# Optimization experiments

Measured on AMD Instinct MI355X. Metric: run time of the kernel, lower is better.

Reference implementation:

```python
import jax, jax.numpy as jnp
import numpy as np

DIM = 1024
D_STATE = 16

def setup_inputs() -> dict:
    key = jax.random.key(0)
    kx, ka, kd = jax.random.split(key, 3)
    x = jax.random.normal(kx, (4, 8192, DIM), dtype=jnp.float32)
    A = jax.random.normal(ka, (DIM, D_STATE), dtype=jnp.float32)
    D = jax.random.normal(kd, (D_STATE, DIM), dtype=jnp.float32)
    return {"x": x, "A": A, "D": D}

def reference(x, A, D):
    # x: [B, N, C]; A: [C, S]; D: [S, C]
    x_state = jnp.einsum('bnc,cs->bns', x, A)        # [B, N, S]
    x_state = jnp.cumsum(x_state, axis=1)            # prefix sum over sequence
    out = jnp.einsum('bns,sc->bnc', x_state, D)      # [B, N, C]
    return out
```

## Files before the change

### kernel.cpp

```cpp
#include <hip/hip_runtime.h>

#define DIM   1024
#define DST   16
#define NSEQ  8192
#define NB    4

#define MT    64
#define KC    128
#define KCP   132
#define NTILE 128

__global__ __launch_bounds__(256) void kA_gemm_scan(
    const float* __restrict__ x, const float* __restrict__ A,
    float* __restrict__ Tloc, float* __restrict__ TS)
{
    __shared__ float xs[MT * KCP];
    __shared__ float at[DST * KCP];
    __shared__ float scanbuf[16 * DST];

    const int t    = threadIdx.x;
    const int b    = blockIdx.x >> 7;
    const int tile = blockIdx.x & 127;
    const int n0   = tile * MT;
    const int s    = t & 15;
    const int mg   = t >> 4;

    const float* xrow = x + ((long)(b * NSEQ + n0)) * DIM;

    float acc0 = 0.f, acc1 = 0.f, acc2 = 0.f, acc3 = 0.f;

    for (int kc = 0; kc < DIM; kc += KC) {
        {
            const int q  = t & 31;
            const int r0 = t >> 5;
            #pragma unroll
            for (int it = 0; it < 8; ++it) {
                const int m = it * 8 + r0;
                const float4 v = *(const float4*)(xrow + (long)m * DIM + kc + 4 * q);
                *(float4*)&xs[m * KCP + 4 * q] = v;
            }
        }
        {
            #pragma unroll
            for (int it = 0; it < 8; ++it) {
                const int idx = it * 256 + t;
                const int kl  = idx >> 4;
                const int ss  = idx & 15;
                at[ss * KCP + kl] = A[(kc + kl) * DST + ss];
            }
        }
        __syncthreads();

        #pragma unroll 4
        for (int kq = 0; kq < KC / 4; ++kq) {
            const float4 a  = *(const float4*)&at[s * KCP + 4 * kq];
            const float4 x0 = *(const float4*)&xs[(mg * 4 + 0) * KCP + 4 * kq];
            const float4 x1 = *(const float4*)&xs[(mg * 4 + 1) * KCP + 4 * kq];
            const float4 x2 = *(const float4*)&xs[(mg * 4 + 2) * KCP + 4 * kq];
            const float4 x3 = *(const float4*)&xs[(mg * 4 + 3) * KCP + 4 * kq];
            acc0 += x0.x * a.x + x0.y * a.y + x0.z * a.z + x0.w * a.w;
            acc1 += x1.x * a.x + x1.y * a.y + x1.z * a.z + x1.w * a.w;
            acc2 += x2.x * a.x + x2.y * a.y + x2.z * a.z + x2.w * a.w;
            acc3 += x3.x * a.x + x3.y * a.y + x3.z * a.z + x3.w * a.w;
        }
        __syncthreads();
    }

    const float rsum = acc0 + acc1 + acc2 + acc3;
    scanbuf[mg * DST + s] = rsum;
    __syncthreads();
    float excl = 0.f, total = 0.f;
    #pragma unroll
    for (int m = 0; m < 16; ++m) {
        const float v = scanbuf[m * DST + s];
        total += v;
        excl  += (m < mg) ? v : 0.f;
    }
    if (mg == 0) TS[((long)b * NTILE + tile) * DST + s] = total;

    const float c0 = excl + acc0;
    const float c1 = c0 + acc1;
    const float c2 = c1 + acc2;
    const float c3 = c2 + acc3;
    *(float4*)&Tloc[((long)(b * DST + s)) * NSEQ + n0 + mg * 4] =
        make_float4(c0, c1, c2, c3);
}

__global__ __launch_bounds__(256) void kB_scan_out(
    const float* __restrict__ Tloc, const float* __restrict__ TS,
    const float* __restrict__ D, float* __restrict__ out)
{
    __shared__ float sp[MT * 20];
    __shared__ float partial[16 * DST];
    __shared__ float basebuf[DST];

    const int t    = threadIdx.x;
    const int b    = blockIdx.x >> 7;
    const int tile = blockIdx.x & 127;
    const int n0   = tile * MT;
    const int s    = t & 15;
    const int mg   = t >> 4;

    float4 dreg[16];
    #pragma unroll
    for (int ss = 0; ss < 16; ++ss)
        dreg[ss] = *(const float4*)&D[ss * DIM + 4 * t];

    {
        const float* tsb = TS + (long)b * NTILE * DST;
        float p = 0.f;
        for (int j = mg; j < tile; j += 16) p += tsb[j * DST + s];
        partial[mg * DST + s] = p;
    }
    __syncthreads();
    {
        float bsum = 0.f;
        #pragma unroll
        for (int m = 0; m < 16; ++m) bsum += partial[m * DST + s];
        if (mg == 0) basebuf[s] = bsum;
    }
    __syncthreads();

    #pragma unroll
    for (int j = 0; j < 4; ++j) {
        const int idx = j * 256 + t;
        const int ss  = idx >> 6;
        const int nn  = idx & 63;
        sp[nn * 20 + ss] = Tloc[((long)(b * DST + ss)) * NSEQ + n0 + nn] + basebuf[ss];
    }
    __syncthreads();

    float* ob = out + ((long)(b * NSEQ + n0)) * DIM + 4 * t;
    for (int r = 0; r < MT; ++r) {
        const float4 s0 = *(const float4*)&sp[r * 20 + 0];
        const float4 s1 = *(const float4*)&sp[r * 20 + 4];
        const float4 s2 = *(const float4*)&sp[r * 20 + 8];
        const float4 s3 = *(const float4*)&sp[r * 20 + 12];
        const float sv[16] = {s0.x, s0.y, s0.z, s0.w, s1.x, s1.y, s1.z, s1.w,
                              s2.x, s2.y, s2.z, s2.w, s3.x, s3.y, s3.z, s3.w};
        float4 o = make_float4(0.f, 0.f, 0.f, 0.f);
        #pragma unroll
        for (int ss = 0; ss < 16; ++ss) {
            o.x += sv[ss] * dreg[ss].x;
            o.y += sv[ss] * dreg[ss].y;
            o.z += sv[ss] * dreg[ss].z;
            o.w += sv[ss] * dreg[ss].w;
        }
        *(float4*)(ob + (long)r * DIM) = o;
    }
}

extern "C" void kernel_launch(void* const* d_in, const int* in_sizes, int n_in,
                              void* d_out, int out_size, void* d_ws, size_t ws_size,
                              hipStream_t stream) {
    const float* x = (const float*)d_in[0];
    const float* A = (const float*)d_in[1];
    const float* D = (const float*)d_in[2];
    float* out  = (float*)d_out;
    float* Tloc = (float*)d_ws;
    float* TS   = Tloc + (long)NB * DST * NSEQ;

    kA_gemm_scan<<<dim3(NB * NTILE), dim3(256), 0, stream>>>(x, A, Tloc, TS);
    kB_scan_out <<<dim3(NB * NTILE), dim3(256), 0, stream>>>(Tloc, TS, D, out);
}
```

Before: 269.6 us.

## Register-tile GEMM in scan kernel with split-K and XOR-swizzled x tile

Reworks the x·A inner loop of the first kernel so each thread computes a 4-row by 4-state register tile over a quarter of the K chunk. This raises arithmetic reuse per shared-memory load. The x tile drops its padding and uses an XOR swizzle to avoid bank conflicts. A shared-memory reduction across the four K groups follows before the existing block scan. The cost is extra registers, an extra reduction pass and added synchronisation.

```diff
diff --git a/kernel.cpp b/kernel.cpp
--- a/kernel.cpp
+++ b/kernel.cpp
@@ -14,7 +14,7 @@
     const float* __restrict__ x, const float* __restrict__ A,
     float* __restrict__ Tloc, float* __restrict__ TS)
 {
-    __shared__ float xs[MT * KCP];
+    __shared__ float xs[MT * KC];
     __shared__ float at[DST * KCP];
     __shared__ float scanbuf[16 * DST];
 
@@ -22,12 +22,20 @@
     const int b    = blockIdx.x >> 7;
     const int tile = blockIdx.x & 127;
     const int n0   = tile * MT;
-    const int s    = t & 15;
-    const int mg   = t >> 4;
+
+    const int kq4 = t >> 6;
+    const int mg  = (t >> 2) & 15;
+    const int sp  = t & 3;
 
     const float* xrow = x + ((long)(b * NSEQ + n0)) * DIM;
 
-    float acc0 = 0.f, acc1 = 0.f, acc2 = 0.f, acc3 = 0.f;
+    float acc[4][4];
+    #pragma unroll
+    for (int r = 0; r < 4; ++r)
+        #pragma unroll
+        for (int j = 0; j < 4; ++j) acc[r][j] = 0.f;
+
+    const int kbase = kq4 * 32;
 
     for (int kc = 0; kc < DIM; kc += KC) {
         {
@@ -35,9 +43,10 @@
             const int r0 = t >> 5;
             #pragma unroll
             for (int it = 0; it < 8; ++it) {
-                const int m = it * 8 + r0;
+                const int m  = it * 8 + r0;
                 const float4 v = *(const float4*)(xrow + (long)m * DIM + kc + 4 * q);
-                *(float4*)&xs[m * KCP + 4 * q] = v;
+                const int qs = q ^ ((m >> 2) & 7);
+                *(float4*)&xs[m * KC + 4 * qs] = v;
             }
         }
         {
@@ -51,38 +60,64 @@
         }
         __syncthreads();
 
-        #pragma unroll 4
-        for (int kq = 0; kq < KC / 4; ++kq) {
-            const float4 a  = *(const float4*)&at[s * KCP + 4 * kq];
-            const float4 x0 = *(const float4*)&xs[(mg * 4 + 0) * KCP + 4 * kq];
-            const float4 x1 = *(const float4*)&xs[(mg * 4 + 1) * KCP + 4 * kq];
-            const float4 x2 = *(const float4*)&xs[(mg * 4 + 2) * KCP + 4 * kq];
-            const float4 x3 = *(const float4*)&xs[(mg * 4 + 3) * KCP + 4 * kq];
-            acc0 += x0.x * a.x + x0.y * a.y + x0.z * a.z + x0.w * a.w;
-            acc1 += x1.x * a.x + x1.y * a.y + x1.z * a.z + x1.w * a.w;
-            acc2 += x2.x * a.x + x2.y * a.y + x2.z * a.z + x2.w * a.w;
-            acc3 += x3.x * a.x + x3.y * a.y + x3.z * a.z + x3.w * a.w;
+        #pragma unroll
+        for (int kq = 0; kq < 8; ++kq) {
+            const int kqi = (kbase >> 2) + kq;
+            const float4 a0 = *(const float4*)&at[(sp +  0) * KCP + kbase + 4 * kq];
+            const float4 a1 = *(const float4*)&at[(sp +  4) * KCP + kbase + 4 * kq];
+            const float4 a2 = *(const float4*)&at[(sp +  8) * KCP + kbase + 4 * kq];
+            const float4 a3 = *(const float4*)&at[(sp + 12) * KCP + kbase + 4 * kq];
+            const int qs = kqi ^ (mg & 7);
+            #pragma unroll
+            for (int r = 0; r < 4; ++r) {
+                const float4 xv = *(const float4*)&xs[(mg * 4 + r) * KC + 4 * qs];
+                acc[r][0] += xv.x * a0.x + xv.y * a0.y + xv.z * a0.z + xv.w * a0.w;
+                acc[r][1] += xv.x * a1.x + xv.y * a1.y + xv.z * a1.z + xv.w * a1.w;
+                acc[r][2] += xv.x * a2.x + xv.y * a2.y + xv.z * a2.z + xv.w * a2.w;
+                acc[r][3] += xv.x * a3.x + xv.y * a3.y + xv.z * a3.z + xv.w * a3.w;
+            }
         }
         __syncthreads();
     }
 
+    float* red = xs;
+    #pragma unroll
+    for (int r = 0; r < 4; ++r)
+        #pragma unroll
+        for (int j = 0; j < 4; ++j)
+            red[kq4 * (64 * 17) + (mg * 4 + r) * 17 + (sp + 4 * j)] = acc[r][j];
+    __syncthreads();
+
+    const int s   = t & 15;
+    const int mg2 = t >> 4;
+    float acc0 = 0.f, acc1 = 0.f, acc2 = 0.f, acc3 = 0.f;
+    #pragma unroll
+    for (int q = 0; q < 4; ++q) {
+        const float* rq = red + q * (64 * 17) + (mg2 * 4) * 17 + s;
+        acc0 += rq[0 * 17];
+        acc1 += rq[1 * 17];
+        acc2 += rq[2 * 17];
+        acc3 += rq[3 * 17];
+    }
+    __syncthreads();
+
     const float rsum = acc0 + acc1 + acc2 + acc3;
-    scanbuf[mg * DST + s] = rsum;
+    scanbuf[mg2 * DST + s] = rsum;
     __syncthreads();
     float excl = 0.f, total = 0.f;
     #pragma unroll
     for (int m = 0; m < 16; ++m) {
         const float v = scanbuf[m * DST + s];
         total += v;
-        excl  += (m < mg) ? v : 0.f;
-    }
-    if (mg == 0) TS[((long)b * NTILE + tile) * DST + s] = total;
+        excl  += (m < mg2) ? v : 0.f;
+    }
+    if (mg2 == 0) TS[((long)b * NTILE + tile) * DST + s] = total;
 
     const float c0 = excl + acc0;
     const float c1 = c0 + acc1;
     const float c2 = c1 + acc2;
     const float c3 = c2 + acc3;
-    *(float4*)&Tloc[((long)(b * DST + s)) * NSEQ + n0 + mg * 4] =
+    *(float4*)&Tloc[((long)(b * DST + s)) * NSEQ + n0 + mg2 * 4] =
         make_float4(c0, c1, c2, c3);
 }
 
```

Result: no change. 271.1 us (+0.6%).

## Double-buffer x tiles via direct global-to-LDS loads with XOR swizzle

Applied to the files above, without the earlier changes.

Kernel A now loads x chunks straight into LDS using global_load_lds with a double buffer, so the next 64-wide K chunk streams in while the current one is computed. LDS rows are XOR-swizzled instead of padded to avoid bank conflicts, and the chunk size drops from 128 to 64. This targets the serialized load-then-compute pattern of the memory-bound first GEMM, at the cost of more loop iterations and reliance on the async LDS load path.

```diff
diff --git a/kernel.cpp b/kernel.cpp
--- a/kernel.cpp
+++ b/kernel.cpp
@@ -6,16 +6,17 @@
 #define NB    4
 
 #define MT    64
-#define KC    128
-#define KCP   132
+#define KC2   64
+#define NCH   16
+#define ATP   68
 #define NTILE 128
 
 __global__ __launch_bounds__(256) void kA_gemm_scan(
     const float* __restrict__ x, const float* __restrict__ A,
     float* __restrict__ Tloc, float* __restrict__ TS)
 {
-    __shared__ float xs[MT * KCP];
-    __shared__ float at[DST * KCP];
+    __shared__ float xs[2][MT * KC2];
+    __shared__ float at[2][DST * ATP];
     __shared__ float scanbuf[16 * DST];
 
     const int t    = threadIdx.x;
@@ -24,45 +25,59 @@
     const int n0   = tile * MT;
     const int s    = t & 15;
     const int mg   = t >> 4;
+    const int w    = t >> 6;
+    const int l    = t & 63;
 
     const float* xrow = x + ((long)(b * NSEQ + n0)) * DIM;
 
     float acc0 = 0.f, acc1 = 0.f, acc2 = 0.f, acc3 = 0.f;
 
-    for (int kc = 0; kc < DIM; kc += KC) {
-        {
-            const int q  = t & 31;
-            const int r0 = t >> 5;
-            #pragma unroll
-            for (int it = 0; it < 8; ++it) {
-                const int m = it * 8 + r0;
-                const float4 v = *(const float4*)(xrow + (long)m * DIM + kc + 4 * q);
-                *(float4*)&xs[m * KCP + 4 * q] = v;
-            }
+    auto stage = [&](int c, int bb) {
+        const int kc = c * KC2;
+        #pragma unroll
+        for (int i = 0; i < 4; ++i) {
+            const int g   = w * 4 + i;
+            const int row = 4 * g + (l >> 4);
+            const int q   = l & 15;
+            const float* src = xrow + (long)row * DIM + kc + 4 * (q ^ (g & 7));
+            __builtin_amdgcn_global_load_lds(
+                (const __attribute__((address_space(1))) void*)src,
+                (__attribute__((address_space(3))) void*)&xs[bb][g * 256],
+                16, 0, 0);
         }
-        {
-            #pragma unroll
-            for (int it = 0; it < 8; ++it) {
-                const int idx = it * 256 + t;
-                const int kl  = idx >> 4;
-                const int ss  = idx & 15;
-                at[ss * KCP + kl] = A[(kc + kl) * DST + ss];
-            }
+        #pragma unroll
+        for (int it = 0; it < 4; ++it) {
+            const int idx = it * 256 + t;
+            const int kl  = idx >> 4;
+            const int ss  = idx & 15;
+            at[bb][ss * ATP + kl] = A[(kc + kl) * DST + ss];
         }
-        __syncthreads();
+    };
 
-        #pragma unroll 4
-        for (int kq = 0; kq < KC / 4; ++kq) {
-            const float4 a  = *(const float4*)&at[s * KCP + 4 * kq];
-            const float4 x0 = *(const float4*)&xs[(mg * 4 + 0) * KCP + 4 * kq];
-            const float4 x1 = *(const float4*)&xs[(mg * 4 + 1) * KCP + 4 * kq];
-            const float4 x2 = *(const float4*)&xs[(mg * 4 + 2) * KCP + 4 * kq];
-            const float4 x3 = *(const float4*)&xs[(mg * 4 + 3) * KCP + 4 * kq];
+    auto compute = [&](int bb) {
+        const float* xb = xs[bb];
+        const float* ab = at[bb];
+        #pragma unroll
+        for (int kq = 0; kq < KC2 / 4; ++kq) {
+            const float4 a  = *(const float4*)&ab[s * ATP + 4 * kq];
+            const int   qp = 4 * (kq ^ (mg & 7));
+            const float4 x0 = *(const float4*)&xb[(mg * 4 + 0) * KC2 + qp];
+            const float4 x1 = *(const float4*)&xb[(mg * 4 + 1) * KC2 + qp];
+            const float4 x2 = *(const float4*)&xb[(mg * 4 + 2) * KC2 + qp];
+            const float4 x3 = *(const float4*)&xb[(mg * 4 + 3) * KC2 + qp];
             acc0 += x0.x * a.x + x0.y * a.y + x0.z * a.z + x0.w * a.w;
             acc1 += x1.x * a.x + x1.y * a.y + x1.z * a.z + x1.w * a.w;
             acc2 += x2.x * a.x + x2.y * a.y + x2.z * a.z + x2.w * a.w;
             acc3 += x3.x * a.x + x3.y * a.y + x3.z * a.z + x3.w * a.w;
         }
+    };
+
+    stage(0, 0);
+    __syncthreads();
+    for (int c = 0; c < NCH; ++c) {
+        const int cur = c & 1;
+        if (c + 1 < NCH) stage(c + 1, cur ^ 1);
+        compute(cur);
         __syncthreads();
     }
 
```

New measurement: 303.0 us. 1.12x slower.

## Use bf16 MFMA for the x·A projection with register-prefetched x rows

Applied to the files above, without the earlier changes.

Replaces the LDS-staged fp32 dot-product GEMM in the first kernel with bf16 MFMA 16x16x32 instructions. x is read straight from global memory into registers with a two-step prefetch, and A is converted to bf16 and transposed into LDS once per block. The MFMA output is redistributed through LDS to match the existing scan layout. This removes the per-chunk LDS staging of x and the scalar FMA work, at the cost of bf16 rounding in a 1024-long reduction whose error then accumulates through the cumsum.

```diff
diff --git a/kernel.cpp b/kernel.cpp
--- a/kernel.cpp
+++ b/kernel.cpp
@@ -6,67 +6,85 @@
 #define NB    4
 
 #define MT    64
-#define KC    128
-#define KCP   132
 #define NTILE 128
+#define ATP   1032
+
+typedef __attribute__((ext_vector_type(8))) short bf16x8;
+typedef __attribute__((ext_vector_type(4))) float f32x4;
+
+__device__ __forceinline__ unsigned short bfc(float f) {
+    const unsigned u = __builtin_bit_cast(unsigned, f);
+    return (unsigned short)((u + 0x7FFFu + ((u >> 16) & 1u)) >> 16);
+}
+
+__device__ __forceinline__ bf16x8 cvt8(float4 a, float4 b) {
+    bf16x8 r;
+    r[0] = (short)bfc(a.x); r[1] = (short)bfc(a.y);
+    r[2] = (short)bfc(a.z); r[3] = (short)bfc(a.w);
+    r[4] = (short)bfc(b.x); r[5] = (short)bfc(b.y);
+    r[6] = (short)bfc(b.z); r[7] = (short)bfc(b.w);
+    return r;
+}
 
 __global__ __launch_bounds__(256) void kA_gemm_scan(
     const float* __restrict__ x, const float* __restrict__ A,
     float* __restrict__ Tloc, float* __restrict__ TS)
 {
-    __shared__ float xs[MT * KCP];
-    __shared__ float at[DST * KCP];
+    __shared__ unsigned short atb[DST * ATP];
+    __shared__ float red[MT * 20];
     __shared__ float scanbuf[16 * DST];
 
     const int t    = threadIdx.x;
     const int b    = blockIdx.x >> 7;
     const int tile = blockIdx.x & 127;
     const int n0   = tile * MT;
-    const int s    = t & 15;
-    const int mg   = t >> 4;
+    const int w    = t >> 6;
+    const int l    = t & 63;
+    const int lm   = l & 15;
+    const int lg   = l >> 4;
 
-    const float* xrow = x + ((long)(b * NSEQ + n0)) * DIM;
+    const float* xp = x + ((long)(b * NSEQ + n0 + w * 16 + lm)) * DIM + lg * 8;
 
-    float acc0 = 0.f, acc1 = 0.f, acc2 = 0.f, acc3 = 0.f;
+    float4 xa0 = *(const float4*)(xp + 0);
+    float4 xa1 = *(const float4*)(xp + 4);
+    float4 xb0 = *(const float4*)(xp + 32);
+    float4 xb1 = *(const float4*)(xp + 36);
 
-    for (int kc = 0; kc < DIM; kc += KC) {
-        {
-            const int q  = t & 31;
-            const int r0 = t >> 5;
-            #pragma unroll
-            for (int it = 0; it < 8; ++it) {
-                const int m = it * 8 + r0;
-                const float4 v = *(const float4*)(xrow + (long)m * DIM + kc + 4 * q);
-                *(float4*)&xs[m * KCP + 4 * q] = v;
-            }
+    #pragma unroll
+    for (int it = 0; it < 64; ++it) {
+        const int idx = it * 256 + t;
+        atb[(idx & 15) * ATP + (idx >> 4)] = bfc(A[idx]);
+    }
+    __syncthreads();
+
+    const int aoff = lm * ATP + lg * 8;
+
+    f32x4 acc = {0.f, 0.f, 0.f, 0.f};
+    #pragma unroll
+    for (int c = 0; c < 32; ++c) {
+        const bf16x8 af = cvt8(xa0, xa1);
+        xa0 = xb0; xa1 = xb1;
+        if (c + 2 < 32) {
+            xb0 = *(const float4*)(xp + 32 * (c + 2));
+            xb1 = *(const float4*)(xp + 32 * (c + 2) + 4);
         }
-        {
-            #pragma unroll
-            for (int it = 0; it < 8; ++it) {
-                const int idx = it * 256 + t;
-                const int kl  = idx >> 4;
-                const int ss  = idx & 15;
-                at[ss * KCP + kl] = A[(kc + kl) * DST + ss];
-            }
-        }
-        __syncthreads();
-
-        #pragma unroll 4
-        for (int kq = 0; kq < KC / 4; ++kq) {
-            const float4 a  = *(const float4*)&at[s * KCP + 4 * kq];
-            const float4 x0 = *(const float4*)&xs[(mg * 4 + 0) * KCP + 4 * kq];
-            const float4 x1 = *(const float4*)&xs[(mg * 4 + 1) * KCP + 4 * kq];
-            const float4 x2 = *(const float4*)&xs[(mg * 4 + 2) * KCP + 4 * kq];
-            const float4 x3 = *(const float4*)&xs[(mg * 4 + 3) * KCP + 4 * kq];
-            acc0 += x0.x * a.x + x0.y * a.y + x0.z * a.z + x0.w * a.w;
-            acc1 += x1.x * a.x + x1.y * a.y + x1.z * a.z + x1.w * a.w;
-            acc2 += x2.x * a.x + x2.y * a.y + x2.z * a.z + x2.w * a.w;
-            acc3 += x3.x * a.x + x3.y * a.y + x3.z * a.z + x3.w * a.w;
-        }
-        __syncthreads();
+        const bf16x8 bfr = *(const bf16x8*)&atb[aoff + 32 * c];
+        acc = __builtin_amdgcn_mfma_f32_16x16x32_bf16(af, bfr, acc, 0, 0, 0);
     }
 
-    const float rsum = acc0 + acc1 + acc2 + acc3;
+    #pragma unroll
+    for (int r = 0; r < 4; ++r)
+        red[(w * 16 + lg * 4 + r) * 20 + lm] = acc[r];
+    __syncthreads();
+
+    const int s  = t & 15;
+    const int mg = t >> 4;
+    const float a0 = red[(mg * 4 + 0) * 20 + s];
+    const float a1 = red[(mg * 4 + 1) * 20 + s];
+    const float a2 = red[(mg * 4 + 2) * 20 + s];
+    const float a3 = red[(mg * 4 + 3) * 20 + s];
+
+    const float rsum = a0 + a1 + a2 + a3;
     scanbuf[mg * DST + s] = rsum;
     __syncthreads();
     float excl = 0.f, total = 0.f;
@@ -78,10 +96,10 @@
     }
     if (mg == 0) TS[((long)b * NTILE + tile) * DST + s] = total;
 
-    const float c0 = excl + acc0;
-    const float c1 = c0 + acc1;
-    const float c2 = c1 + acc2;
-    const float c3 = c2 + acc3;
+    const float c0 = excl + a0;
+    const float c1 = c0 + a1;
+    const float c2 = c1 + a2;
+    const float c3 = c2 + a3;
     *(float4*)&Tloc[((long)(b * DST + s)) * NSEQ + n0 + mg * 4] =
         make_float4(c0, c1, c2, c3);
 }
```

New measurement: 274.7 us. No clear change (+1.9%).
